# Kernel optimization log

Measured on AMD Instinct MI355X. Metric: run time of the kernel, lower is better.

## Reference

```python
import jax, jax.numpy as jnp
import numpy as np

DIM = 1024
DIM_HEAD = 64
HEADS = 16
BATCH = 2
SEQ = 2048
SCALE = DIM_HEAD ** -0.5


def setup_inputs() -> dict:
    key = jax.random.key(0)
    ks = jax.random.split(key, 5)
    tokens = jax.random.normal(ks[0], (BATCH, SEQ, DIM), dtype=jnp.float32)
    wq = jax.random.normal(ks[1], (HEADS, DIM, DIM_HEAD), dtype=jnp.float32)
    wk = jax.random.normal(ks[2], (HEADS, DIM, DIM_HEAD), dtype=jnp.float32)
    wv = jax.random.normal(ks[3], (HEADS, DIM, DIM_HEAD), dtype=jnp.float32)
    wo = jax.random.normal(ks[4], (HEADS, DIM_HEAD, DIM), dtype=jnp.float32)
    return {"tokens": tokens, "wq": wq, "wk": wk, "wv": wv, "wo": wo}


def reference(tokens, wq, wk, wv, wo):
    # q, k, v: [b, h, n, dh]
    q = jnp.einsum('bnd,hde->bhne', tokens, wq) * SCALE
    k = jnp.einsum('bnd,hde->bhne', tokens, wk)
    v = jnp.einsum('bnd,hde->bhne', tokens, wv)
    sim = jnp.einsum('bhie,bhje->bhij', q, k)          # [b, h, n, n]
    attn = jax.nn.softmax(sim, axis=-1)
    aggregated = jnp.einsum('bhij,bhje->bhie', attn, v)  # [b, h, n, dh]
    retrieved = jnp.einsum('bhne,hed->bnd', aggregated, wo)  # sum over heads
    return retrieved
```

## Files before the change

### kernel.cpp

```cpp
#include <hip/hip_runtime.h>
#include <hip/hip_fp16.h>

#define BB 2
#define HH 16
#define SS 2048
#define DD 1024
#define DHH 64
#define QSCALE 0.18033688011112042f

typedef _Float16 half8 __attribute__((ext_vector_type(8)));
typedef _Float16 half4 __attribute__((ext_vector_type(4)));
typedef __fp16 fp16x2 __attribute__((ext_vector_type(2)));
typedef float floatx4 __attribute__((ext_vector_type(4)));

__device__ __forceinline__ floatx4 mfma16(half8 a, half8 b, floatx4 c) {
  return __builtin_amdgcn_mfma_f32_16x16x32_f16(a, b, c, 0, 0, 0);
}

__global__ __launch_bounds__(256) void convert_kernel(
    const float* __restrict__ wq, const float* __restrict__ wk,
    const float* __restrict__ wv, const float* __restrict__ wo,
    _Float16* __restrict__ Wh, _Float16* __restrict__ Wl,
    _Float16* __restrict__ Wot)
{
  __shared__ float St[64][68];
  const int kt = blockIdx.x;
  const int hy = blockIdx.y;
  const int z  = blockIdx.z;
  const int t  = (int)threadIdx.x;
  const int k0 = kt * 64;

  const float* src = (z == 0) ? (wq + hy * (DD * DHH))
                   : (z == 1) ? (wk + hy * (DD * DHH))
                   : (z == 2) ? (wv + hy * (DD * DHH))
                   : wo;

  const int rr = t >> 4, cc = (t & 15) * 4;
  if (z < 3) {
    #pragma unroll
    for (int i = 0; i < 4; ++i)
      *(floatx4*)&St[rr + 16 * i][cc] =
          *(const floatx4*)(src + (k0 + rr + 16 * i) * DHH + cc);
  } else {
    const int d0 = hy * 64;
    #pragma unroll
    for (int i = 0; i < 4; ++i)
      *(floatx4*)&St[rr + 16 * i][cc] =
          *(const floatx4*)(src + (k0 + rr + 16 * i) * 1024 + d0 + cc);
  }
  __syncthreads();

  const int e = t >> 2, kc = (t & 3) * 16;
  if (z < 3) {
    const int n = z * 1024 + hy * 64 + e;
    half8 hi0, hi1, lo0, lo1;
    #pragma unroll
    for (int u = 0; u < 16; ++u) {
      float x = St[kc + u][e];
      _Float16 hh = (_Float16)x;
      _Float16 ll = (_Float16)(x - (float)hh);
      if (u < 8) { hi0[u] = hh; lo0[u] = ll; }
      else       { hi1[u - 8] = hh; lo1[u - 8] = ll; }
    }
    *(half8*)(Wh + n * 1024 + k0 + kc)     = hi0;
    *(half8*)(Wh + n * 1024 + k0 + kc + 8) = hi1;
    *(half8*)(Wl + n * 1024 + k0 + kc)     = lo0;
    *(half8*)(Wl + n * 1024 + k0 + kc + 8) = lo1;
  } else {
    const int d0 = hy * 64;
    half8 hi0, hi1;
    #pragma unroll
    for (int u = 0; u < 16; ++u) {
      _Float16 hh = (_Float16)St[kc + u][e];
      if (u < 8) hi0[u] = hh; else hi1[u - 8] = hh;
    }
    *(half8*)(Wot + (d0 + e) * 1024 + k0 + kc)     = hi0;
    *(half8*)(Wot + (d0 + e) * 1024 + k0 + kc + 8) = hi1;
  }
}

__global__ __launch_bounds__(256) void tokens_split_kernel(
    const float* __restrict__ tokens,
    _Float16* __restrict__ th, _Float16* __restrict__ tl)
{
  const int i = ((int)blockIdx.x * 256 + (int)threadIdx.x) * 8;
  floatx4 x0 = *(const floatx4*)(tokens + i);
  floatx4 x1 = *(const floatx4*)(tokens + i + 4);
  half8 h, l;
  #pragma unroll
  for (int j = 0; j < 8; ++j) {
    float x = (j < 4) ? x0[j] : x1[j - 4];
    _Float16 hh = (_Float16)x;
    h[j] = hh;
    l[j] = (_Float16)(x - (float)hh);
  }
  *(half8*)(th + i) = h;
  *(half8*)(tl + i) = l;
}

__global__ __launch_bounds__(256) void qkv_gemm_kernel(
    const _Float16* __restrict__ th, const _Float16* __restrict__ tl,
    const _Float16* __restrict__ Wh, const _Float16* __restrict__ Wl,
    _Float16* __restrict__ qh, _Float16* __restrict__ ql,
    _Float16* __restrict__ kh, _Float16* __restrict__ kl,
    _Float16* __restrict__ vt)
{
  __shared__ _Float16 Ah[128][40], Al[128][40], Bh[128][40], Bl[128][40];
  const int n0 = blockIdx.x * 128;
  const int m0 = blockIdx.y * 128;
  const int zb = n0 >> 10;
  const bool is_v = (zb == 2);
  const int t = (int)threadIdx.x;
  const int lane = t & 63, wid = t >> 6;
  const int l16 = lane & 15, q4 = lane >> 4;
  const int mw = (wid & 1) * 64, nw = (wid >> 1) * 64;

  const int r0 = t >> 2, kc0 = (t & 3) * 8;
  const int r1 = (t + 256) >> 2, kc1 = kc0;

  const floatx4 z4 = {0.0f, 0.0f, 0.0f, 0.0f};
  floatx4 acc[4][4];
  #pragma unroll
  for (int mi = 0; mi < 4; ++mi)
    #pragma unroll
    for (int ni = 0; ni < 4; ++ni) acc[mi][ni] = z4;

  half8 pA0, pA1, pL0, pL1, pB0, pB1, pC0, pC1;
  const _Float16* thp = th + m0 * 1024;
  const _Float16* tlp = tl + m0 * 1024;
  const _Float16* Whp = Wh + n0 * 1024;
  const _Float16* Wlp = Wl + n0 * 1024;

  {
    pA0 = *(const half8*)(thp + r0 * 1024 + kc0);
    pA1 = *(const half8*)(thp + r1 * 1024 + kc1);
    if (!is_v) {
      pL0 = *(const half8*)(tlp + r0 * 1024 + kc0);
      pL1 = *(const half8*)(tlp + r1 * 1024 + kc1);
    }
    pB0 = *(const half8*)(Whp + r0 * 1024 + kc0);
    pB1 = *(const half8*)(Whp + r1 * 1024 + kc1);
    pC0 = *(const half8*)(Wlp + r0 * 1024 + kc0);
    pC1 = *(const half8*)(Wlp + r1 * 1024 + kc1);
  }

  for (int kt = 0; kt < 32; ++kt) {
    __syncthreads();
    *(half8*)&Ah[r0][kc0] = pA0;
    *(half8*)&Ah[r1][kc1] = pA1;
    if (!is_v) {
      *(half8*)&Al[r0][kc0] = pL0;
      *(half8*)&Al[r1][kc1] = pL1;
    }
    *(half8*)&Bh[r0][kc0] = pB0;
    *(half8*)&Bh[r1][kc1] = pB1;
    *(half8*)&Bl[r0][kc0] = pC0;
    *(half8*)&Bl[r1][kc1] = pC1;
    __syncthreads();

    if (kt < 31) {
      const int ko = (kt + 1) * 32;
      pA0 = *(const half8*)(thp + r0 * 1024 + ko + kc0);
      pA1 = *(const half8*)(thp + r1 * 1024 + ko + kc1);
      if (!is_v) {
        pL0 = *(const half8*)(tlp + r0 * 1024 + ko + kc0);
        pL1 = *(const half8*)(tlp + r1 * 1024 + ko + kc1);
      }
      pB0 = *(const half8*)(Whp + r0 * 1024 + ko + kc0);
      pB1 = *(const half8*)(Whp + r1 * 1024 + ko + kc1);
      pC0 = *(const half8*)(Wlp + r0 * 1024 + ko + kc0);
      pC1 = *(const half8*)(Wlp + r1 * 1024 + ko + kc1);
    }

    half8 a_h[4];
    #pragma unroll
    for (int mi = 0; mi < 4; ++mi)
      a_h[mi] = *(const half8*)&Ah[mw + mi * 16 + l16][q4 * 8];
    if (!is_v) {
      half8 a_l[4];
      #pragma unroll
      for (int mi = 0; mi < 4; ++mi)
        a_l[mi] = *(const half8*)&Al[mw + mi * 16 + l16][q4 * 8];
      #pragma unroll
      for (int ni = 0; ni < 4; ++ni) {
        const half8 b_h = *(const half8*)&Bh[nw + ni * 16 + l16][q4 * 8];
        const half8 b_l = *(const half8*)&Bl[nw + ni * 16 + l16][q4 * 8];
        #pragma unroll
        for (int mi = 0; mi < 4; ++mi) {
          acc[mi][ni] = mfma16(a_h[mi], b_h, acc[mi][ni]);
          acc[mi][ni] = mfma16(a_h[mi], b_l, acc[mi][ni]);
          acc[mi][ni] = mfma16(a_l[mi], b_h, acc[mi][ni]);
        }
      }
    } else {
      #pragma unroll
      for (int ni = 0; ni < 4; ++ni) {
        const half8 b_h = *(const half8*)&Bh[nw + ni * 16 + l16][q4 * 8];
        const half8 b_l = *(const half8*)&Bl[nw + ni * 16 + l16][q4 * 8];
        #pragma unroll
        for (int mi = 0; mi < 4; ++mi) {
          acc[mi][ni] = mfma16(a_h[mi], b_h, acc[mi][ni]);
          acc[mi][ni] = mfma16(a_h[mi], b_l, acc[mi][ni]);
        }
      }
    }
  }

  #pragma unroll
  for (int ni = 0; ni < 4; ++ni) {
    const int ncol = n0 + nw + ni * 16;
    const int h = (ncol >> 6) & 15;
    const int e = (ncol & 63) + l16;
    #pragma unroll
    for (int mi = 0; mi < 4; ++mi) {
      #pragma unroll
      for (int r = 0; r < 4; ++r) {
        const int grow = m0 + mw + mi * 16 + q4 * 4 + r;
        const int b = grow >> 11, s = grow & 2047;
        const float v = acc[mi][ni][r];
        const int qkidx = ((b * HH + h) * SS + s) * DHH + e;
        if (zb == 0) {
          const float vs = v * QSCALE;
          const _Float16 hh = (_Float16)vs;
          qh[qkidx] = hh;
          ql[qkidx] = (_Float16)(vs - (float)hh);
        } else if (zb == 1) {
          const _Float16 hh = (_Float16)v;
          kh[qkidx] = hh;
          kl[qkidx] = (_Float16)(v - (float)hh);
        } else {
          vt[((b * HH + h) * DHH + e) * SS + s] = (_Float16)v;
        }
      }
    }
  }
}

__global__ __launch_bounds__(512) void attn_kernel(
    const _Float16* __restrict__ qh, const _Float16* __restrict__ ql,
    const _Float16* __restrict__ kh, const _Float16* __restrict__ kl,
    const _Float16* __restrict__ vt, _Float16* __restrict__ agg)
{
  __shared__ _Float16 Kh[64][72], Kl[64][72], Vs[64][72];
  __shared__ _Float16 Ps[128][72];

  const int qt = blockIdx.x;
  const int h  = blockIdx.y;
  const int b  = blockIdx.z;
  const int bh = b * HH + h;
  const int t = (int)threadIdx.x;
  const int lane = t & 63, wid = t >> 6;
  const int l16 = lane & 15, q4 = lane >> 4;

  const int sr = t >> 3, sc = (t & 7) * 8;

  half8 qfh[2], qfl[2];
  {
    const int s = qt * 128 + wid * 16 + l16;
    const int base = (bh * SS + s) * DHH + q4 * 8;
    qfh[0] = *(const half8*)(qh + base);
    qfh[1] = *(const half8*)(qh + base + 32);
    qfl[0] = *(const half8*)(ql + base);
    qfl[1] = *(const half8*)(ql + base + 32);
  }

  const floatx4 z4 = {0.0f, 0.0f, 0.0f, 0.0f};
  floatx4 o[4];
  #pragma unroll
  for (int i = 0; i < 4; ++i) o[i] = z4;
  float m_r = -1e30f, l_r = 0.0f;

  half8 pK, pL, pV;
  {
    const int gk = (bh * SS + sr) * DHH + sc;
    pK = *(const half8*)(kh + gk);
    pL = *(const half8*)(kl + gk);
    pV = *(const half8*)(vt + (bh * DHH + sr) * SS + sc);
  }

  for (int kt = 0; kt < 32; ++kt) {
    __syncthreads();
    *(half8*)&Kh[sr][sc] = pK;
    *(half8*)&Kl[sr][sc] = pL;
    *(half8*)&Vs[sr][sc] = pV;
    __syncthreads();

    if (kt < 31) {
      const int k1 = (kt + 1) * 64;
      const int gk = (bh * SS + k1 + sr) * DHH + sc;
      pK = *(const half8*)(kh + gk);
      pL = *(const half8*)(kl + gk);
      pV = *(const half8*)(vt + (bh * DHH + sr) * SS + k1 + sc);
    }

    floatx4 sv[4];
    #pragma unroll
    for (int sub = 0; sub < 4; ++sub) {
      const half8 ah0 = *(const half8*)&Kh[sub * 16 + l16][q4 * 8];
      const half8 ah1 = *(const half8*)&Kh[sub * 16 + l16][q4 * 8 + 32];
      const half8 al0 = *(const half8*)&Kl[sub * 16 + l16][q4 * 8];
      const half8 al1 = *(const half8*)&Kl[sub * 16 + l16][q4 * 8 + 32];
      floatx4 s4 = z4;
      s4 = mfma16(ah0, qfh[0], s4);
      s4 = mfma16(ah1, qfh[1], s4);
      s4 = mfma16(al0, qfh[0], s4);
      s4 = mfma16(al1, qfh[1], s4);
      s4 = mfma16(ah0, qfl[0], s4);
      s4 = mfma16(ah1, qfl[1], s4);
      sv[sub] = s4;
    }

    float mx = fmaxf(fmaxf(sv[0][0], sv[0][1]), fmaxf(sv[0][2], sv[0][3]));
    #pragma unroll
    for (int sub = 1; sub < 4; ++sub)
      mx = fmaxf(mx, fmaxf(fmaxf(sv[sub][0], sv[sub][1]),
                           fmaxf(sv[sub][2], sv[sub][3])));
    mx = fmaxf(mx, __shfl_xor(mx, 16));
    mx = fmaxf(mx, __shfl_xor(mx, 32));
    const float mnew = fmaxf(m_r, mx);

    float psum = 0.0f;
    #pragma unroll
    for (int sub = 0; sub < 4; ++sub) {
      #pragma unroll
      for (int r = 0; r < 4; ++r) {
        float p = exp2f(sv[sub][r] - mnew);
        sv[sub][r] = p;
        psum += p;
      }
    }

    #pragma unroll
    for (int sub = 0; sub < 4; ++sub) {
      fp16x2 p01 = __builtin_amdgcn_cvt_pkrtz(sv[sub][0], sv[sub][1]);
      fp16x2 p23 = __builtin_amdgcn_cvt_pkrtz(sv[sub][2], sv[sub][3]);
      half4 pv;
      pv[0] = (_Float16)p01[0]; pv[1] = (_Float16)p01[1];
      pv[2] = (_Float16)p23[0]; pv[3] = (_Float16)p23[1];
      *(half4*)&Ps[wid * 16 + l16][sub * 16 + q4 * 4] = pv;
    }

    psum += __shfl_xor(psum, 16);
    psum += __shfl_xor(psum, 32);

    if (__any(mnew > m_r)) {
      const float alpha = exp2f(m_r - mnew);
      l_r = l_r * alpha + psum;
      m_r = mnew;
      #pragma unroll
      for (int sub = 0; sub < 4; ++sub)
        #pragma unroll
        for (int r = 0; r < 4; ++r) o[sub][r] *= alpha;
    } else {
      l_r += psum;
    }

    asm volatile("s_waitcnt lgkmcnt(0)" ::: "memory");

    const half8 pb0 = *(const half8*)&Ps[wid * 16 + l16][q4 * 8];
    const half8 pb1 = *(const half8*)&Ps[wid * 16 + l16][q4 * 8 + 32];
    #pragma unroll
    for (int sub = 0; sub < 4; ++sub) {
      const half8 va0 = *(const half8*)&Vs[sub * 16 + l16][q4 * 8];
      const half8 va1 = *(const half8*)&Vs[sub * 16 + l16][q4 * 8 + 32];
      o[sub] = mfma16(va0, pb0, o[sub]);
      o[sub] = mfma16(va1, pb1, o[sub]);
    }
  }

  const float inv = 1.0f / l_r;
  const int s = qt * 128 + wid * 16 + l16;
  #pragma unroll
  for (int sub = 0; sub < 4; ++sub) {
    half4 ov;
    #pragma unroll
    for (int r = 0; r < 4; ++r) ov[r] = (_Float16)(o[sub][r] * inv);
    *(half4*)(agg + (b * SS + s) * (HH * DHH) + h * DHH + sub * 16 + q4 * 4) = ov;
  }
}

__global__ __launch_bounds__(256) void out_gemm_kernel(
    const _Float16* __restrict__ agg, const _Float16* __restrict__ Wot,
    float* __restrict__ out)
{
  __shared__ _Float16 As[128][40], Bs[128][40];
  const int n0 = blockIdx.x * 128;
  const int m0 = blockIdx.y * 128;
  const int t = (int)threadIdx.x;
  const int lane = t & 63, wid = t >> 6;
  const int l16 = lane & 15, q4 = lane >> 4;
  const int mw = (wid & 1) * 64, nw = (wid >> 1) * 64;

  const floatx4 z4 = {0.0f, 0.0f, 0.0f, 0.0f};
  floatx4 acc[4][4];
  #pragma unroll
  for (int mi = 0; mi < 4; ++mi)
    #pragma unroll
    for (int ni = 0; ni < 4; ++ni) acc[mi][ni] = z4;

  for (int kt = 0; kt < 32; ++kt) {
    __syncthreads();
    #pragma unroll
    for (int j = 0; j < 2; ++j) {
      const int idx = t + 256 * j;
      const int r = idx >> 2, kc = (idx & 3) * 8;
      *(half8*)&As[r][kc] = *(const half8*)(agg + (m0 + r) * 1024 + kt * 32 + kc);
      *(half8*)&Bs[r][kc] = *(const half8*)(Wot + (n0 + r) * 1024 + kt * 32 + kc);
    }
    __syncthreads();

    half8 a_f[4];
    #pragma unroll
    for (int mi = 0; mi < 4; ++mi)
      a_f[mi] = *(const half8*)&As[mw + mi * 16 + l16][q4 * 8];
    #pragma unroll
    for (int ni = 0; ni < 4; ++ni) {
      const half8 b_f = *(const half8*)&Bs[nw + ni * 16 + l16][q4 * 8];
      #pragma unroll
      for (int mi = 0; mi < 4; ++mi)
        acc[mi][ni] = mfma16(a_f[mi], b_f, acc[mi][ni]);
    }
  }

  #pragma unroll
  for (int ni = 0; ni < 4; ++ni)
    #pragma unroll
    for (int mi = 0; mi < 4; ++mi)
      #pragma unroll
      for (int r = 0; r < 4; ++r)
        out[(m0 + mw + mi * 16 + q4 * 4 + r) * 1024 + n0 + nw + ni * 16 + l16] =
            acc[mi][ni][r];
}

extern "C" void kernel_launch(void* const* d_in, const int* in_sizes, int n_in,
                              void* d_out, int out_size, void* d_ws, size_t ws_size,
                              hipStream_t stream)
{
  const float* tokens = (const float*)d_in[0];
  const float* wq = (const float*)d_in[1];
  const float* wk = (const float*)d_in[2];
  const float* wv = (const float*)d_in[3];
  const float* wo = (const float*)d_in[4];
  float* out = (float*)d_out;

  char* ws = (char*)d_ws;
  _Float16* qh  = (_Float16*)(ws);
  _Float16* ql  = (_Float16*)(ws + 8388608);
  _Float16* kh  = (_Float16*)(ws + 16777216);
  _Float16* kl  = (_Float16*)(ws + 25165824);
  _Float16* vt  = (_Float16*)(ws + 33554432);
  _Float16* Wh  = (_Float16*)(ws + 41943040);
  _Float16* Wl  = (_Float16*)(ws + 48234496);
  _Float16* Wot = (_Float16*)(ws + 54525952);
  _Float16* th  = (_Float16*)(ws + 56623104);
  _Float16* tl  = (_Float16*)(ws + 65011712);
  _Float16* agg = (_Float16*)(ws + 56623104);

  convert_kernel<<<dim3(16, 16, 4), 256, 0, stream>>>(wq, wk, wv, wo, Wh, Wl, Wot);
  tokens_split_kernel<<<2048, 256, 0, stream>>>(tokens, th, tl);
  qkv_gemm_kernel<<<dim3(24, 32), 256, 0, stream>>>(th, tl, Wh, Wl, qh, ql, kh, kl, vt);
  attn_kernel<<<dim3(16, 16, 2), 512, 0, stream>>>(qh, ql, kh, kl, vt, agg);
  out_gemm_kernel<<<dim3(8, 32), 256, 0, stream>>>(agg, Wot, out);
}
```

Baseline: 292.6 us.

## Stage QKV and output GEMM tiles via direct global-to-LDS loads with XOR swizzle

Replaces the register-staged global loads and LDS stores in the QKV and output projection GEMMs with global_load_lds DMA (16-byte per lane). Each wave now loads one operand tile, using an XOR-swizzled, unpadded LDS layout to avoid bank conflicts. The aim is to cut VGPR pressure and the LDS write instructions. The cost is that the register prefetch of the next k-tile is removed, so global load latency is exposed between the barriers.

```diff
diff --git a/kernel.cpp b/kernel.cpp
--- a/kernel.cpp
+++ b/kernel.cpp
@@ -1,5 +1,6 @@
 #include <hip/hip_runtime.h>
 #include <hip/hip_fp16.h>
+#include <stdint.h>
 
 #define BB 2
 #define HH 16
@@ -16,6 +17,14 @@
 __device__ __forceinline__ floatx4 mfma16(half8 a, half8 b, floatx4 c) {
   return __builtin_amdgcn_mfma_f32_16x16x32_f16(a, b, c, 0, 0, 0);
 }
+
+__device__ __forceinline__ void dma16(const _Float16* g, _Float16* l) {
+  __builtin_amdgcn_global_load_lds(
+      (const __attribute__((address_space(1))) uint32_t*)g,
+      (__attribute__((address_space(3))) uint32_t*)l,
+      16, 0, 0);
+}
+
 
 __global__ __launch_bounds__(256) void convert_kernel(
     const float* __restrict__ wq, const float* __restrict__ wk,
@@ -105,7 +114,11 @@
     _Float16* __restrict__ kh, _Float16* __restrict__ kl,
     _Float16* __restrict__ vt)
 {
-  __shared__ _Float16 Ah[128][40], Al[128][40], Bh[128][40], Bl[128][40];
+  __shared__ alignas(16) _Float16 sAh[128 * 32];
+  __shared__ alignas(16) _Float16 sAl[128 * 32];
+  __shared__ alignas(16) _Float16 sBh[128 * 32];
+  __shared__ alignas(16) _Float16 sBl[128 * 32];
+
   const int n0 = blockIdx.x * 128;
   const int m0 = blockIdx.y * 128;
   const int zb = n0 >> 10;
@@ -115,8 +128,20 @@
   const int l16 = lane & 15, q4 = lane >> 4;
   const int mw = (wid & 1) * 64, nw = (wid >> 1) * 64;
 
-  const int r0 = t >> 2, kc0 = (t & 3) * 8;
-  const int r1 = (t + 256) >> 2, kc1 = kc0;
+  const int g  = (lane & 7) ^ ((lane >> 3) & 7);
+  const int grow  = (lane >> 3) * 2 + (g >> 2);
+  const int gcol8 = (g & 3) * 8;
+
+  const int laneoff = (l16 >> 1) * 128 + (((((l16 & 1) << 2) | q4) ^ (l16 >> 1)) * 16);
+
+  const _Float16* src;
+  _Float16* dst;
+  if (wid == 0)      { src = th + m0 * 1024; dst = sAh; }
+  else if (wid == 1) { src = Wh + n0 * 1024; dst = sBh; }
+  else if (wid == 2) { src = Wl + n0 * 1024; dst = sBl; }
+  else               { src = tl + m0 * 1024; dst = sAl; }
+  const bool stage_active = !(is_v && wid == 3);
+  const _Float16* gsrc = src + grow * 1024 + gcol8;
 
   const floatx4 z4 = {0.0f, 0.0f, 0.0f, 0.0f};
   floatx4 acc[4][4];
@@ -125,66 +150,29 @@
     #pragma unroll
     for (int ni = 0; ni < 4; ++ni) acc[mi][ni] = z4;
 
-  half8 pA0, pA1, pL0, pL1, pB0, pB1, pC0, pC1;
-  const _Float16* thp = th + m0 * 1024;
-  const _Float16* tlp = tl + m0 * 1024;
-  const _Float16* Whp = Wh + n0 * 1024;
-  const _Float16* Wlp = Wl + n0 * 1024;
-
-  {
-    pA0 = *(const half8*)(thp + r0 * 1024 + kc0);
-    pA1 = *(const half8*)(thp + r1 * 1024 + kc1);
-    if (!is_v) {
-      pL0 = *(const half8*)(tlp + r0 * 1024 + kc0);
-      pL1 = *(const half8*)(tlp + r1 * 1024 + kc1);
-    }
-    pB0 = *(const half8*)(Whp + r0 * 1024 + kc0);
-    pB1 = *(const half8*)(Whp + r1 * 1024 + kc1);
-    pC0 = *(const half8*)(Wlp + r0 * 1024 + kc0);
-    pC1 = *(const half8*)(Wlp + r1 * 1024 + kc1);
-  }
-
   for (int kt = 0; kt < 32; ++kt) {
     __syncthreads();
-    *(half8*)&Ah[r0][kc0] = pA0;
-    *(half8*)&Ah[r1][kc1] = pA1;
-    if (!is_v) {
-      *(half8*)&Al[r0][kc0] = pL0;
-      *(half8*)&Al[r1][kc1] = pL1;
-    }
-    *(half8*)&Bh[r0][kc0] = pB0;
-    *(half8*)&Bh[r1][kc1] = pB1;
-    *(half8*)&Bl[r0][kc0] = pC0;
-    *(half8*)&Bl[r1][kc1] = pC1;
-    __syncthreads();
-
-    if (kt < 31) {
-      const int ko = (kt + 1) * 32;
-      pA0 = *(const half8*)(thp + r0 * 1024 + ko + kc0);
-      pA1 = *(const half8*)(thp + r1 * 1024 + ko + kc1);
-      if (!is_v) {
-        pL0 = *(const half8*)(tlp + r0 * 1024 + ko + kc0);
-        pL1 = *(const half8*)(tlp + r1 * 1024 + ko + kc1);
-      }
-      pB0 = *(const half8*)(Whp + r0 * 1024 + ko + kc0);
-      pB1 = *(const half8*)(Whp + r1 * 1024 + ko + kc1);
-      pC0 = *(const half8*)(Wlp + r0 * 1024 + ko + kc0);
-      pC1 = *(const half8*)(Wlp + r1 * 1024 + ko + kc1);
-    }
+    if (stage_active) {
+      const _Float16* gp = gsrc + kt * 32;
+      #pragma unroll
+      for (int j = 0; j < 8; ++j)
+        dma16(gp + j * 16 * 1024, dst + j * 16 * 32);
+    }
+    __syncthreads();
 
     half8 a_h[4];
     #pragma unroll
     for (int mi = 0; mi < 4; ++mi)
-      a_h[mi] = *(const half8*)&Ah[mw + mi * 16 + l16][q4 * 8];
+      a_h[mi] = *(const half8*)((const char*)sAh + (mw + mi * 16) * 64 + laneoff);
     if (!is_v) {
       half8 a_l[4];
       #pragma unroll
       for (int mi = 0; mi < 4; ++mi)
-        a_l[mi] = *(const half8*)&Al[mw + mi * 16 + l16][q4 * 8];
+        a_l[mi] = *(const half8*)((const char*)sAl + (mw + mi * 16) * 64 + laneoff);
       #pragma unroll
       for (int ni = 0; ni < 4; ++ni) {
-        const half8 b_h = *(const half8*)&Bh[nw + ni * 16 + l16][q4 * 8];
-        const half8 b_l = *(const half8*)&Bl[nw + ni * 16 + l16][q4 * 8];
+        const half8 b_h = *(const half8*)((const char*)sBh + (nw + ni * 16) * 64 + laneoff);
+        const half8 b_l = *(const half8*)((const char*)sBl + (nw + ni * 16) * 64 + laneoff);
         #pragma unroll
         for (int mi = 0; mi < 4; ++mi) {
           acc[mi][ni] = mfma16(a_h[mi], b_h, acc[mi][ni]);
@@ -195,8 +183,8 @@
     } else {
       #pragma unroll
       for (int ni = 0; ni < 4; ++ni) {
-        const half8 b_h = *(const half8*)&Bh[nw + ni * 16 + l16][q4 * 8];
-        const half8 b_l = *(const half8*)&Bl[nw + ni * 16 + l16][q4 * 8];
+        const half8 b_h = *(const half8*)((const char*)sBh + (nw + ni * 16) * 64 + laneoff);
+        const half8 b_l = *(const half8*)((const char*)sBl + (nw + ni * 16) * 64 + laneoff);
         #pragma unroll
         for (int mi = 0; mi < 4; ++mi) {
           acc[mi][ni] = mfma16(a_h[mi], b_h, acc[mi][ni]);
@@ -215,8 +203,8 @@
     for (int mi = 0; mi < 4; ++mi) {
       #pragma unroll
       for (int r = 0; r < 4; ++r) {
-        const int grow = m0 + mw + mi * 16 + q4 * 4 + r;
-        const int b = grow >> 11, s = grow & 2047;
+        const int grow2 = m0 + mw + mi * 16 + q4 * 4 + r;
+        const int b = grow2 >> 11, s = grow2 & 2047;
         const float v = acc[mi][ni][r];
         const int qkidx = ((b * HH + h) * SS + s) * DHH + e;
         if (zb == 0) {
@@ -383,7 +371,8 @@
     const _Float16* __restrict__ agg, const _Float16* __restrict__ Wot,
     float* __restrict__ out)
 {
-  __shared__ _Float16 As[128][40], Bs[128][40];
+  __shared__ alignas(16) _Float16 sA[128 * 32];
+  __shared__ alignas(16) _Float16 sB[128 * 32];
   const int n0 = blockIdx.x * 128;
   const int m0 = blockIdx.y * 128;
   const int t = (int)threadIdx.x;
@@ -391,6 +380,17 @@
   const int l16 = lane & 15, q4 = lane >> 4;
   const int mw = (wid & 1) * 64, nw = (wid >> 1) * 64;
 
+  const int g  = (lane & 7) ^ ((lane >> 3) & 7);
+  const int grow  = (lane >> 3) * 2 + (g >> 2);
+  const int gcol8 = (g & 3) * 8;
+  const int laneoff = (l16 >> 1) * 128 + (((((l16 & 1) << 2) | q4) ^ (l16 >> 1)) * 16);
+
+  const _Float16* src = (wid < 2) ? (agg + m0 * 1024) : (Wot + n0 * 1024);
+  _Float16* dst = (wid < 2) ? sA : sB;
+  const int half64 = (wid & 1) * 64;
+  const _Float16* gsrc = src + (half64 + grow) * 1024 + gcol8;
+  _Float16* ldst = dst + half64 * 32;
+
   const floatx4 z4 = {0.0f, 0.0f, 0.0f, 0.0f};
   floatx4 acc[4][4];
   #pragma unroll
@@ -400,22 +400,21 @@
 
   for (int kt = 0; kt < 32; ++kt) {
     __syncthreads();
-    #pragma unroll
-    for (int j = 0; j < 2; ++j) {
-      const int idx = t + 256 * j;
-      const int r = idx >> 2, kc = (idx & 3) * 8;
-      *(half8*)&As[r][kc] = *(const half8*)(agg + (m0 + r) * 1024 + kt * 32 + kc);
-      *(half8*)&Bs[r][kc] = *(const half8*)(Wot + (n0 + r) * 1024 + kt * 32 + kc);
+    {
+      const _Float16* gp = gsrc + kt * 32;
+      #pragma unroll
+      for (int j = 0; j < 4; ++j)
+        dma16(gp + j * 16 * 1024, ldst + j * 16 * 32);
     }
     __syncthreads();
 
     half8 a_f[4];
     #pragma unroll
     for (int mi = 0; mi < 4; ++mi)
-      a_f[mi] = *(const half8*)&As[mw + mi * 16 + l16][q4 * 8];
+      a_f[mi] = *(const half8*)((const char*)sA + (mw + mi * 16) * 64 + laneoff);
     #pragma unroll
     for (int ni = 0; ni < 4; ++ni) {
-      const half8 b_f = *(const half8*)&Bs[nw + ni * 16 + l16][q4 * 8];
+      const half8 b_f = *(const half8*)((const char*)sB + (nw + ni * 16) * 64 + laneoff);
       #pragma unroll
       for (int mi = 0; mi < 4; ++mi)
         acc[mi][ni] = mfma16(a_f[mi], b_f, acc[mi][ni]);
```

Measured after the change: 303.8 us. 3.8% more time.
